# Performance work log

Measured on AMD Instinct MI355X. Metric: run time of the kernel, lower is better.

## Reference

```python
import jax, jax.numpy as jnp
import numpy as np

B, S, D = 1, 2048, 1024   # batch, seq, hidden_size
I = 2048                  # intermediate_size (mlp1 emits 2*I, SwiGLU halves)
E = 8                     # num_experts
K = 2                     # experts_per_token
LIMIT = 7.0               # swiglu_limit
ALPHA = 1.702             # gpt-oss swiglu alpha
EPS = 1e-5                # RMSNorm eps


def setup_inputs() -> dict:
    key = jax.random.key(0)
    ks = jax.random.split(key, 4)
    s = 0.02
    return {
        "x": jax.random.normal(ks[0], (B, S, D), jnp.float32),
        "norm_scale": jnp.ones((D,), jnp.float32),
        "gate_w": jax.random.normal(ks[1], (D, E), jnp.float32) * s,
        "gate_b": jnp.zeros((E,), jnp.float32),
        "mlp1_w": jax.random.normal(ks[2], (E, D, 2 * I), jnp.float32) * s,
        "mlp1_b": jnp.zeros((E, 2 * I), jnp.float32),
        "mlp2_w": jax.random.normal(ks[3], (E, I, D), jnp.float32) * s,
        "mlp2_b": jnp.zeros((E, D), jnp.float32),
    }


def _swiglu(h):
    # gpt-oss interleaved SwiGLU with clamp limit
    x_glu = jnp.minimum(h[..., ::2], LIMIT)
    x_lin = jnp.clip(h[..., 1::2], -LIMIT, LIMIT)
    return x_glu * jax.nn.sigmoid(ALPHA * x_glu) * (x_lin + 1.0)


def _moe(t, gate_w, gate_b, mlp1_w, mlp1_b, mlp2_w, mlp2_b):
    T = t.shape[0]
    logits = t @ gate_w + gate_b                 # [T, E]
    top_v, top_i = jax.lax.top_k(logits, K)      # [T, K]
    probs = jax.nn.softmax(top_v, axis=-1)       # softmax over selected experts
    # dense routing-weight matrix, zero for unselected experts
    w = jnp.zeros((T, E), t.dtype).at[jnp.arange(T)[:, None], top_i].set(probs)

    def body(acc, ew):
        w1, b1, w2, b2, we = ew                  # per-expert params + weights [T]
        h = _swiglu(t @ w1 + b1)                 # [T, I]
        y = h @ w2 + b2                          # [T, D]
        return acc + we[:, None] * y, None

    acc0 = jnp.zeros((T, t.shape[1]), t.dtype)
    acc, _ = jax.lax.scan(body, acc0, (mlp1_w, mlp1_b, mlp2_w, mlp2_b, w.T))
    return acc


def reference(x, norm_scale, gate_w, gate_b, mlp1_w, mlp1_b, mlp2_w, mlp2_b):
    Bx, Sx, Dx = x.shape
    ms = jnp.mean(x * x, axis=-1, keepdims=True)
    t = (x * jax.lax.rsqrt(ms + EPS) * norm_scale).reshape(Bx * Sx, Dx)
    y = _moe(t, gate_w, gate_b, mlp1_w, mlp1_b, mlp2_w, mlp2_b)
    return x + y.reshape(Bx, Sx, Dx)
```

## Files before the change

### kernel.cpp

```cpp
#include <hip/hip_runtime.h>
#include <hip/hip_bf16.h>

typedef unsigned short u16;
typedef __attribute__((ext_vector_type(4))) unsigned short u16x4;
typedef __attribute__((ext_vector_type(8))) unsigned short u16x8;
typedef __attribute__((ext_vector_type(8))) short bf16x8;
typedef __attribute__((ext_vector_type(4))) float f32x4;

#define DEV static __device__ __forceinline__

DEV float bf2f(u16 b){ union{unsigned u; float f;} c; c.u = ((unsigned)b) << 16; return c.f; }
DEV u16 f2bf(float f){ union{float f; unsigned u;} c; c.f = f; unsigned u = c.u; u += 0x7FFF + ((u >> 16) & 1); return (u16)(u >> 16); }
DEV u16 f2bfh(float f){ union { __hip_bfloat16 h; u16 u; } c; c.h = __float2bfloat16(f); return c.u; }
DEV float getc(float4 v, int c){ return c == 0 ? v.x : c == 1 ? v.y : c == 2 ? v.z : v.w; }

DEV void gload16(const void* g, void* l){
  __builtin_amdgcn_global_load_lds((const __attribute__((address_space(1))) unsigned int*)g,
                                   (__attribute__((address_space(3))) unsigned int*)l, 16, 0, 0);
}

__global__ __launch_bounds__(256) void k_rms(
    const float* __restrict__ x, const float* __restrict__ nsc,
    const float* __restrict__ gw, const float* __restrict__ gb,
    u16* __restrict__ t, int* __restrict__ topi, float* __restrict__ topp)
{
  const int token = blockIdx.x, tid = threadIdx.x;
  const int wv = tid >> 6, lane = tid & 63;
  const float4 xv = *(const float4*)&x[(size_t)token * 1024 + tid * 4];
  float f[4] = {xv.x, xv.y, xv.z, xv.w};
  float ss = f[0]*f[0] + f[1]*f[1] + f[2]*f[2] + f[3]*f[3];
  #pragma unroll
  for (int o = 32; o > 0; o >>= 1) ss += __shfl_down(ss, o, 64);
  __shared__ float red[4];
  __shared__ float s_rs;
  if (lane == 0) red[wv] = ss;
  __syncthreads();
  if (tid == 0) s_rs = rsqrtf((red[0] + red[1] + red[2] + red[3]) * (1.0f / 1024.0f) + 1e-5f);
  __syncthreads();
  const float rs = s_rs;
  const float4 sv = *(const float4*)&nsc[tid * 4];
  const float sc[4] = {sv.x, sv.y, sv.z, sv.w};
  float tf[4]; u16x4 tv;
  #pragma unroll
  for (int j = 0; j < 4; ++j){ tf[j] = f[j] * rs * sc[j]; tv[j] = f2bf(tf[j]); }
  *(u16x4*)&t[(size_t)token * 1024 + tid * 4] = tv;

  float la[8] = {0,0,0,0,0,0,0,0};
  #pragma unroll
  for (int j = 0; j < 4; ++j){
    const int k = tid * 4 + j;
    const float4 g0 = *(const float4*)&gw[k * 8];
    const float4 g1 = *(const float4*)&gw[k * 8 + 4];
    la[0] += tf[j] * g0.x; la[1] += tf[j] * g0.y; la[2] += tf[j] * g0.z; la[3] += tf[j] * g0.w;
    la[4] += tf[j] * g1.x; la[5] += tf[j] * g1.y; la[6] += tf[j] * g1.z; la[7] += tf[j] * g1.w;
  }
  #pragma unroll
  for (int o = 32; o > 0; o >>= 1)
    #pragma unroll
    for (int e = 0; e < 8; ++e) la[e] += __shfl_down(la[e], o, 64);
  __shared__ float lred[4][8];
  if (lane == 0){
    #pragma unroll
    for (int e = 0; e < 8; ++e) lred[wv][e] = la[e];
  }
  __syncthreads();
  if (tid == 0){
    float lg[8];
    #pragma unroll
    for (int e = 0; e < 8; ++e) lg[e] = lred[0][e] + lred[1][e] + lred[2][e] + lred[3][e] + gb[e];
    int i0 = 0;
    for (int e = 1; e < 8; ++e) if (lg[e] > lg[i0]) i0 = e;
    int i1 = -1;
    for (int e = 0; e < 8; ++e) if (e != i0 && (i1 < 0 || lg[e] > lg[i1])) i1 = e;
    const float d = __expf(lg[i1] - lg[i0]);
    const float p0 = 1.0f / (1.0f + d);
    topi[token * 2] = i0; topi[token * 2 + 1] = i1;
    topp[token * 2] = p0; topp[token * 2 + 1] = d * p0;
  }
}

__global__ __launch_bounds__(256) void k_route(
    const int* __restrict__ topi, const float* __restrict__ topp,
    int* __restrict__ cnt, int* __restrict__ offs, int* __restrict__ tok_of,
    float* __restrict__ wt_of, int* __restrict__ slot_of, int* __restrict__ posg)
{
  __shared__ int c[8];
  __shared__ int o[8];
  const int tid = threadIdx.x;
  if (tid < 8) c[tid] = 0;
  __syncthreads();
  for (int a = tid; a < 4096; a += 256){
    int e = topi[a];
    posg[a] = atomicAdd(&c[e], 1);
  }
  __syncthreads();
  if (tid == 0){
    int run = 0;
    for (int e = 0; e < 8; ++e){ o[e] = run; offs[e] = run; cnt[e] = c[e]; run += c[e]; }
  }
  __syncthreads();
  for (int a = tid; a < 4096; a += 256){
    int e = topi[a];
    int s = o[e] + posg[a];
    tok_of[s] = a >> 1;
    wt_of[s] = topp[a];
    slot_of[a] = s;
  }
}

__global__ __launch_bounds__(512, 4) void k_gemm1(
    const u16* __restrict__ t, const float* __restrict__ w1, const float* __restrict__ b1,
    const int* __restrict__ cnt, const int* __restrict__ offs, const int* __restrict__ tok_of,
    u16* __restrict__ h)
{
  const int e = blockIdx.z;
  const int count = cnt[e];
  const int m0 = blockIdx.y * 256;
  if (m0 >= count) return;
  const int off = offs[e];
  const int n0 = blockIdx.x * 128;

  __shared__ __attribute__((aligned(16))) u16 As[256 * 64];
  __shared__ __attribute__((aligned(16))) u16 Bs[128 * 64];

  const int tid = threadIdx.x, wv = tid >> 6, lane = tid & 63;
  const int arl = lane >> 3;
  const int axu = (lane & 7) ^ arl;

  const u16* asrc[4];
  u16* adst[4];
  #pragma unroll
  for (int i = 0; i < 4; ++i){
    const int rr = i * 64 + wv * 8 + arl;
    int r = m0 + rr; if (r > count - 1) r = count - 1;
    asrc[i] = t + (size_t)tok_of[off + r] * 1024 + axu * 8;
    adst[i] = &As[(i * 64 + wv * 8) * 64];
  }

  const int tkq = tid >> 5;
  const int tnb = (tid & 31) * 4;
  const float* bsrc = w1 + (size_t)e * (1024 * 4096) + (size_t)(tkq * 4) * 4096 + n0 + tnb;

  const int wm = wv & 3, wn = wv >> 2;
  const int fr = lane & 15, q = lane >> 4;

  f32x4 acc[4][4];
  #pragma unroll
  for (int a = 0; a < 4; ++a)
    #pragma unroll
    for (int b = 0; b < 4; ++b) acc[a][b] = (f32x4){0.f, 0.f, 0.f, 0.f};

  for (int k0 = 0; k0 < 1024; k0 += 64){
    #pragma unroll
    for (int i = 0; i < 4; ++i){ gload16(asrc[i], adst[i]); asrc[i] += 64; }
    const float4 fv0 = *(const float4*)(bsrc);
    const float4 fv1 = *(const float4*)(bsrc + 4096);
    const float4 fv2 = *(const float4*)(bsrc + 2 * 4096);
    const float4 fv3 = *(const float4*)(bsrc + 3 * 4096);
    bsrc += (size_t)64 * 4096;
    #pragma unroll
    for (int c = 0; c < 4; ++c){
      const int nr = tnb + c;
      u16x4 wd;
      wd[0] = f2bfh(getc(fv0, c)); wd[1] = f2bfh(getc(fv1, c));
      wd[2] = f2bfh(getc(fv2, c)); wd[3] = f2bfh(getc(fv3, c));
      *(u16x4*)((char*)Bs + nr * 128 + (((tkq >> 1) ^ ((nr >> 1) & 7)) << 4) + ((tkq & 1) << 3)) = wd;
    }
    __syncthreads();
    #pragma unroll
    for (int hh = 0; hh < 2; ++hh){
      const int puA = (((hh * 4) + q) ^ (fr & 7)) * 8;
      const int puB = (((hh * 4) + q) ^ ((fr >> 1) & 7)) * 8;
      bf16x8 af[4], bq[4];
      #pragma unroll
      for (int fm = 0; fm < 4; ++fm) af[fm] = *(const bf16x8*)&As[(wm * 64 + fm * 16 + fr) * 64 + puA];
      #pragma unroll
      for (int fn = 0; fn < 4; ++fn) bq[fn] = *(const bf16x8*)&Bs[(wn * 64 + fn * 16 + fr) * 64 + puB];
      #pragma unroll
      for (int fm = 0; fm < 4; ++fm)
        #pragma unroll
        for (int fn = 0; fn < 4; ++fn)
          acc[fm][fn] = __builtin_amdgcn_mfma_f32_16x16x32_bf16(af[fm], bq[fn], acc[fm][fn], 0, 0, 0);
    }
    __syncthreads();
  }

  const int cb = n0 + wn * 64 + fr;
  float b1v[4];
  #pragma unroll
  for (int fn = 0; fn < 4; ++fn) b1v[fn] = b1[e * 4096 + cb + fn * 16];
  const int rq = q * 4;
  const bool ev = ((lane & 1) == 0);
  #pragma unroll
  for (int fm = 0; fm < 4; ++fm)
    #pragma unroll
    for (int fn = 0; fn < 4; ++fn)
      #pragma unroll
      for (int r = 0; r < 4; ++r){
        const float val = acc[fm][fn][r] + b1v[fn];
        const float oth = __shfl_xor(val, 1, 64);
        if (ev){
          const int row = m0 + wm * 64 + fm * 16 + rq + r;
          if (row < count){
            const float g = fminf(val, 7.0f);
            const float l = fminf(fmaxf(oth, -7.0f), 7.0f);
            const float o = g / (1.0f + __expf(-1.702f * g)) * (l + 1.0f);
            h[(size_t)(off + row) * 2048 + ((cb + fn * 16) >> 1)] = f2bf(o);
          }
        }
      }
}

__global__ __launch_bounds__(256) void k_gemm2(
    const u16* __restrict__ h, const float* __restrict__ w2, const float* __restrict__ b2,
    const int* __restrict__ cnt, const int* __restrict__ offs, const float* __restrict__ wt_of,
    u16* __restrict__ ys)
{
  const int e = blockIdx.z;
  const int count = cnt[e];
  const int m0 = blockIdx.y * 128;
  if (m0 >= count) return;
  const int off = offs[e];
  const int n0 = blockIdx.x * 64;

  __shared__ __attribute__((aligned(16))) u16 As[2][128 * 64];
  __shared__ __attribute__((aligned(16))) u16 Bs[2][64 * 64];

  const int tid = threadIdx.x, wv = tid >> 6, lane = tid & 63;
  const int arl = lane >> 3;
  const int axu = (lane & 7) ^ arl;

  const u16* asrc[4];
  u16* adst[2][4];
  #pragma unroll
  for (int i = 0; i < 4; ++i){
    const int rr = i * 32 + wv * 8 + arl;
    int r = m0 + rr; if (r > count - 1) r = count - 1;
    asrc[i] = h + (size_t)(off + r) * 2048 + axu * 8;
    adst[0][i] = &As[0][(i * 32 + wv * 8) * 64];
    adst[1][i] = &As[1][(i * 32 + wv * 8) * 64];
  }

  const int tkq = tid >> 4;
  const int tnb = (tid & 15) * 4;
  const float* bsrc = w2 + (size_t)e * (2048 * 1024) + (size_t)(tkq * 4) * 1024 + n0 + tnb;

  const int wm = wv & 1, wn = wv >> 1;
  const int fr = lane & 15, q = lane >> 4;

  f32x4 acc[4][2];
  #pragma unroll
  for (int a = 0; a < 4; ++a)
    #pragma unroll
    for (int b = 0; b < 2; ++b) acc[a][b] = (f32x4){0.f, 0.f, 0.f, 0.f};

  auto loadB = [&](float4* fv){
    #pragma unroll
    for (int j = 0; j < 4; ++j) fv[j] = *(const float4*)(bsrc + (size_t)j * 1024);
    bsrc += (size_t)64 * 1024;
  };
  auto writeB = [&](u16* B, const float4* fv){
    #pragma unroll
    for (int c = 0; c < 4; ++c){
      const int nr = tnb + c;
      u16x4 wd;
      wd[0] = f2bfh(getc(fv[0], c)); wd[1] = f2bfh(getc(fv[1], c));
      wd[2] = f2bfh(getc(fv[2], c)); wd[3] = f2bfh(getc(fv[3], c));
      *(u16x4*)((char*)B + nr * 128 + (((tkq >> 1) ^ ((nr >> 1) & 7)) << 4) + ((tkq & 1) << 3)) = wd;
    }
  };
  auto compute = [&](const u16* A, const u16* B){
    #pragma unroll
    for (int hh = 0; hh < 2; ++hh){
      const int puA = (((hh * 4) + q) ^ (fr & 7)) * 8;
      const int puB = (((hh * 4) + q) ^ ((fr >> 1) & 7)) * 8;
      bf16x8 af[4], bq[2];
      #pragma unroll
      for (int fm = 0; fm < 4; ++fm) af[fm] = *(const bf16x8*)&A[(wm * 64 + fm * 16 + fr) * 64 + puA];
      #pragma unroll
      for (int fn = 0; fn < 2; ++fn) bq[fn] = *(const bf16x8*)&B[(wn * 32 + fn * 16 + fr) * 64 + puB];
      #pragma unroll
      for (int fm = 0; fm < 4; ++fm)
        #pragma unroll
        for (int fn = 0; fn < 2; ++fn)
          acc[fm][fn] = __builtin_amdgcn_mfma_f32_16x16x32_bf16(af[fm], bq[fn], acc[fm][fn], 0, 0, 0);
    }
  };

  {
    #pragma unroll
    for (int i = 0; i < 4; ++i){ gload16(asrc[i], adst[0][i]); asrc[i] += 64; }
    float4 fv[4];
    loadB(fv);
    writeB(Bs[0], fv);
  }
  __syncthreads();

  int cur = 0;
  for (int tt = 0; tt < 31; ++tt){
    const int nxt = cur ^ 1;
    #pragma unroll
    for (int i = 0; i < 4; ++i){ gload16(asrc[i], adst[nxt][i]); asrc[i] += 64; }
    float4 fv[4];
    loadB(fv);
    compute(As[cur], Bs[cur]);
    writeB(Bs[nxt], fv);
    __syncthreads();
    cur = nxt;
  }
  compute(As[cur], Bs[cur]);

  const int cb = n0 + wn * 32 + fr;
  float b2v[2];
  #pragma unroll
  for (int fn = 0; fn < 2; ++fn) b2v[fn] = b2[e * 1024 + cb + fn * 16];
  const int rq = q * 4;
  #pragma unroll
  for (int fm = 0; fm < 4; ++fm)
    #pragma unroll
    for (int rr = 0; rr < 4; ++rr){
      const int row = m0 + wm * 64 + fm * 16 + rq + rr;
      if (row < count){
        const float wt = wt_of[off + row];
        #pragma unroll
        for (int fn = 0; fn < 2; ++fn){
          const float v = (acc[fm][fn][rr] + b2v[fn]) * wt;
          ys[(size_t)(off + row) * 1024 + cb + fn * 16] = f2bf(v);
        }
      }
    }
}

__global__ __launch_bounds__(256) void k_final(
    const float* __restrict__ x, const u16* __restrict__ ys,
    const int* __restrict__ slot_of, float* __restrict__ out)
{
  const int gid = blockIdx.x * 256 + threadIdx.x;
  const int token = gid >> 8;
  const int c0 = (gid & 255) * 4;
  const int s0 = slot_of[token * 2], s1 = slot_of[token * 2 + 1];
  const float4 xv = *(const float4*)&x[(size_t)token * 1024 + c0];
  const u16x4 y0 = *(const u16x4*)&ys[(size_t)s0 * 1024 + c0];
  const u16x4 y1 = *(const u16x4*)&ys[(size_t)s1 * 1024 + c0];
  float4 o;
  o.x = xv.x + bf2f(y0[0]) + bf2f(y1[0]);
  o.y = xv.y + bf2f(y0[1]) + bf2f(y1[1]);
  o.z = xv.z + bf2f(y0[2]) + bf2f(y1[2]);
  o.w = xv.w + bf2f(y0[3]) + bf2f(y1[3]);
  *(float4*)&out[(size_t)token * 1024 + c0] = o;
}

extern "C" void kernel_launch(void* const* d_in, const int* in_sizes, int n_in,
                              void* d_out, int out_size, void* d_ws, size_t ws_size,
                              hipStream_t stream)
{
  const float* x   = (const float*)d_in[0];
  const float* nsc = (const float*)d_in[1];
  const float* gw  = (const float*)d_in[2];
  const float* gb  = (const float*)d_in[3];
  const float* w1  = (const float*)d_in[4];
  const float* b1  = (const float*)d_in[5];
  const float* w2  = (const float*)d_in[6];
  const float* b2  = (const float*)d_in[7];
  float* out = (float*)d_out;
  char* ws = (char*)d_ws;

  size_t o = 0;
  auto alloc = [&](size_t bytes){ size_t r = o; o = (o + bytes + 255) & ~(size_t)255; return r; };
  const size_t o_t    = alloc((size_t)2048 * 1024 * 2);
  const size_t o_h    = alloc((size_t)4096 * 2048 * 2);
  const size_t o_ys   = alloc((size_t)4096 * 1024 * 2);
  const size_t o_topi = alloc(4096 * 4);
  const size_t o_topp = alloc(4096 * 4);
  const size_t o_posg = alloc(4096 * 4);
  const size_t o_tok  = alloc(4096 * 4);
  const size_t o_wt   = alloc(4096 * 4);
  const size_t o_slot = alloc(4096 * 4);
  const size_t o_cnt  = alloc(8 * 4);
  const size_t o_offs = alloc(8 * 4);
  if (ws_size < o) return;

  u16*   t_ws  = (u16*)(ws + o_t);
  u16*   h_ws  = (u16*)(ws + o_h);
  u16*   ys    = (u16*)(ws + o_ys);
  int*   topi  = (int*)(ws + o_topi);
  float* topp  = (float*)(ws + o_topp);
  int*   posg  = (int*)(ws + o_posg);
  int*   tok   = (int*)(ws + o_tok);
  float* wt    = (float*)(ws + o_wt);
  int*   slot  = (int*)(ws + o_slot);
  int*   cnt   = (int*)(ws + o_cnt);
  int*   offs  = (int*)(ws + o_offs);

  k_rms  <<<2048, 256, 0, stream>>>(x, nsc, gw, gb, t_ws, topi, topp);
  k_route<<<1, 256, 0, stream>>>(topi, topp, cnt, offs, tok, wt, slot, posg);
  k_gemm1<<<dim3(32, 4, 8), 512, 0, stream>>>(t_ws, w1, b1, cnt, offs, tok, h_ws);
  k_gemm2<<<dim3(16, 16, 8), 256, 0, stream>>>(h_ws, w2, b2, cnt, offs, wt, ys);
  k_final<<<2048, 256, 0, stream>>>(x, ys, slot, out);
}
```

Baseline: 364.4 us.

## Fuse final combine into gemm2 via atomic adds and load A directly

The residual copy moves into the RMSNorm kernel, which now writes x into the output. gemm2 scatters weighted expert outputs straight into the output with float atomicAdd, which removes the bf16 ys buffer and the k_final kernel. gemm2 also drops its LDS staging of the A (h) tile and reads A fragments from global memory directly into registers each K step. This saves a launch and a round trip through ys. The cost is atomic traffic, non-deterministic summation order, and unpipelined, uncoalesced global A loads that may stall the MFMA loop.

New measurement: 415.4 us. 1.14x slower.

```diff
diff --git a/kernel.cpp b/kernel.cpp
--- a/kernel.cpp
+++ b/kernel.cpp
@@ -22,11 +22,13 @@
 __global__ __launch_bounds__(256) void k_rms(
     const float* __restrict__ x, const float* __restrict__ nsc,
     const float* __restrict__ gw, const float* __restrict__ gb,
-    u16* __restrict__ t, int* __restrict__ topi, float* __restrict__ topp)
+    u16* __restrict__ t, int* __restrict__ topi, float* __restrict__ topp,
+    float* __restrict__ outp)
 {
   const int token = blockIdx.x, tid = threadIdx.x;
   const int wv = tid >> 6, lane = tid & 63;
   const float4 xv = *(const float4*)&x[(size_t)token * 1024 + tid * 4];
+  *(float4*)&outp[(size_t)token * 1024 + tid * 4] = xv;
   float f[4] = {xv.x, xv.y, xv.z, xv.w};
   float ss = f[0]*f[0] + f[1]*f[1] + f[2]*f[2] + f[3]*f[3];
   #pragma unroll
@@ -214,7 +216,7 @@
 __global__ __launch_bounds__(256) void k_gemm2(
     const u16* __restrict__ h, const float* __restrict__ w2, const float* __restrict__ b2,
     const int* __restrict__ cnt, const int* __restrict__ offs, const float* __restrict__ wt_of,
-    u16* __restrict__ ys)
+    const int* __restrict__ tok_of, float* __restrict__ outp)
 {
   const int e = blockIdx.z;
   const int count = cnt[e];
@@ -223,30 +225,23 @@
   const int off = offs[e];
   const int n0 = blockIdx.x * 64;
 
-  __shared__ __attribute__((aligned(16))) u16 As[2][128 * 64];
   __shared__ __attribute__((aligned(16))) u16 Bs[2][64 * 64];
 
   const int tid = threadIdx.x, wv = tid >> 6, lane = tid & 63;
-  const int arl = lane >> 3;
-  const int axu = (lane & 7) ^ arl;
-
-  const u16* asrc[4];
-  u16* adst[2][4];
-  #pragma unroll
-  for (int i = 0; i < 4; ++i){
-    const int rr = i * 32 + wv * 8 + arl;
-    int r = m0 + rr; if (r > count - 1) r = count - 1;
-    asrc[i] = h + (size_t)(off + r) * 2048 + axu * 8;
-    adst[0][i] = &As[0][(i * 32 + wv * 8) * 64];
-    adst[1][i] = &As[1][(i * 32 + wv * 8) * 64];
+  const int wm = wv & 1, wn = wv >> 1;
+  const int fr = lane & 15, q = lane >> 4;
+
+  const u16* abase[4];
+  #pragma unroll
+  for (int fm = 0; fm < 4; ++fm){
+    int r = m0 + wm * 64 + fm * 16 + fr;
+    if (r > count - 1) r = count - 1;
+    abase[fm] = h + (size_t)(off + r) * 2048;
   }
 
   const int tkq = tid >> 4;
   const int tnb = (tid & 15) * 4;
   const float* bsrc = w2 + (size_t)e * (2048 * 1024) + (size_t)(tkq * 4) * 1024 + n0 + tnb;
-
-  const int wm = wv & 1, wn = wv >> 1;
-  const int fr = lane & 15, q = lane >> 4;
 
   f32x4 acc[4][2];
   #pragma unroll
@@ -269,27 +264,28 @@
       *(u16x4*)((char*)B + nr * 128 + (((tkq >> 1) ^ ((nr >> 1) & 7)) << 4) + ((tkq & 1) << 3)) = wd;
     }
   };
-  auto compute = [&](const u16* A, const u16* B){
+  auto computeK = [&](const u16* B, int k0){
+    bf16x8 af[4][2];
+    #pragma unroll
+    for (int fm = 0; fm < 4; ++fm)
+      #pragma unroll
+      for (int hh = 0; hh < 2; ++hh)
+        af[fm][hh] = *(const bf16x8*)(abase[fm] + k0 + (hh * 4 + q) * 8);
     #pragma unroll
     for (int hh = 0; hh < 2; ++hh){
-      const int puA = (((hh * 4) + q) ^ (fr & 7)) * 8;
       const int puB = (((hh * 4) + q) ^ ((fr >> 1) & 7)) * 8;
-      bf16x8 af[4], bq[2];
-      #pragma unroll
-      for (int fm = 0; fm < 4; ++fm) af[fm] = *(const bf16x8*)&A[(wm * 64 + fm * 16 + fr) * 64 + puA];
+      bf16x8 bq[2];
       #pragma unroll
       for (int fn = 0; fn < 2; ++fn) bq[fn] = *(const bf16x8*)&B[(wn * 32 + fn * 16 + fr) * 64 + puB];
       #pragma unroll
       for (int fm = 0; fm < 4; ++fm)
         #pragma unroll
         for (int fn = 0; fn < 2; ++fn)
-          acc[fm][fn] = __builtin_amdgcn_mfma_f32_16x16x32_bf16(af[fm], bq[fn], acc[fm][fn], 0, 0, 0);
+          acc[fm][fn] = __builtin_amdgcn_mfma_f32_16x16x32_bf16(af[fm][hh], bq[fn], acc[fm][fn], 0, 0, 0);
     }
   };
 
   {
-    #pragma unroll
-    for (int i = 0; i < 4; ++i){ gload16(asrc[i], adst[0][i]); asrc[i] += 64; }
     float4 fv[4];
     loadB(fv);
     writeB(Bs[0], fv);
@@ -298,17 +294,14 @@
 
   int cur = 0;
   for (int tt = 0; tt < 31; ++tt){
-    const int nxt = cur ^ 1;
-    #pragma unroll
-    for (int i = 0; i < 4; ++i){ gload16(asrc[i], adst[nxt][i]); asrc[i] += 64; }
     float4 fv[4];
     loadB(fv);
-    compute(As[cur], Bs[cur]);
-    writeB(Bs[nxt], fv);
+    computeK(Bs[cur], tt * 64);
+    writeB(Bs[cur ^ 1], fv);
     __syncthreads();
-    cur = nxt;
-  }
-  compute(As[cur], Bs[cur]);
+    cur ^= 1;
+  }
+  computeK(Bs[cur], 31 * 64);
 
   const int cb = n0 + wn * 32 + fr;
   float b2v[2];
@@ -322,32 +315,14 @@
       const int row = m0 + wm * 64 + fm * 16 + rq + rr;
       if (row < count){
         const float wt = wt_of[off + row];
+        const int token = tok_of[off + row];
         #pragma unroll
         for (int fn = 0; fn < 2; ++fn){
           const float v = (acc[fm][fn][rr] + b2v[fn]) * wt;
-          ys[(size_t)(off + row) * 1024 + cb + fn * 16] = f2bf(v);
+          atomicAdd(&outp[(size_t)token * 1024 + cb + fn * 16], v);
         }
       }
     }
-}
-
-__global__ __launch_bounds__(256) void k_final(
-    const float* __restrict__ x, const u16* __restrict__ ys,
-    const int* __restrict__ slot_of, float* __restrict__ out)
-{
-  const int gid = blockIdx.x * 256 + threadIdx.x;
-  const int token = gid >> 8;
-  const int c0 = (gid & 255) * 4;
-  const int s0 = slot_of[token * 2], s1 = slot_of[token * 2 + 1];
-  const float4 xv = *(const float4*)&x[(size_t)token * 1024 + c0];
-  const u16x4 y0 = *(const u16x4*)&ys[(size_t)s0 * 1024 + c0];
-  const u16x4 y1 = *(const u16x4*)&ys[(size_t)s1 * 1024 + c0];
-  float4 o;
-  o.x = xv.x + bf2f(y0[0]) + bf2f(y1[0]);
-  o.y = xv.y + bf2f(y0[1]) + bf2f(y1[1]);
-  o.z = xv.z + bf2f(y0[2]) + bf2f(y1[2]);
-  o.w = xv.w + bf2f(y0[3]) + bf2f(y1[3]);
-  *(float4*)&out[(size_t)token * 1024 + c0] = o;
 }
 
 extern "C" void kernel_launch(void* const* d_in, const int* in_sizes, int n_in,
@@ -369,7 +344,6 @@
   auto alloc = [&](size_t bytes){ size_t r = o; o = (o + bytes + 255) & ~(size_t)255; return r; };
   const size_t o_t    = alloc((size_t)2048 * 1024 * 2);
   const size_t o_h    = alloc((size_t)4096 * 2048 * 2);
-  const size_t o_ys   = alloc((size_t)4096 * 1024 * 2);
   const size_t o_topi = alloc(4096 * 4);
   const size_t o_topp = alloc(4096 * 4);
   const size_t o_posg = alloc(4096 * 4);
@@ -382,7 +356,6 @@
 
   u16*   t_ws  = (u16*)(ws + o_t);
   u16*   h_ws  = (u16*)(ws + o_h);
-  u16*   ys    = (u16*)(ws + o_ys);
   int*   topi  = (int*)(ws + o_topi);
   float* topp  = (float*)(ws + o_topp);
   int*   posg  = (int*)(ws + o_posg);
@@ -392,9 +365,8 @@
   int*   cnt   = (int*)(ws + o_cnt);
   int*   offs  = (int*)(ws + o_offs);
 
-  k_rms  <<<2048, 256, 0, stream>>>(x, nsc, gw, gb, t_ws, topi, topp);
+  k_rms  <<<2048, 256, 0, stream>>>(x, nsc, gw, gb, t_ws, topi, topp, out);
   k_route<<<1, 256, 0, stream>>>(topi, topp, cnt, offs, tok, wt, slot, posg);
   k_gemm1<<<dim3(32, 4, 8), 512, 0, stream>>>(t_ws, w1, b1, cnt, offs, tok, h_ws);
-  k_gemm2<<<dim3(16, 16, 8), 256, 0, stream>>>(h_ws, w2, b2, cnt, offs, wt, ys);
-  k_final<<<2048, 256, 0, stream>>>(x, ys, slot, out);
-}
+  k_gemm2<<<dim3(16, 16, 8), 256, 0, stream>>>(h_ws, w2, b2, cnt, offs, wt, tok, out);
+}
```
